# Kernel tuning notes

Measured on AMD Instinct MI355X. Metric: run time of the kernel, lower is better.

## Reference

```python
import jax, jax.numpy as jnp
import numpy as np


def setup_inputs() -> dict:
    key = jax.random.key(0)
    ks = jax.random.split(key, 7)
    bs, win_len, num_obj, d = 4, 64, 36, 2048
    s = 1.0 / np.sqrt(d)
    return {
        "region_feats": jax.random.normal(ks[0], (bs, win_len, num_obj, d), jnp.float32),
        "Wq": jax.random.normal(ks[1], (d, d), jnp.float32) * s,
        "bq": jax.random.normal(ks[2], (d,), jnp.float32) * 0.01,
        "Wk": jax.random.normal(ks[3], (d, d), jnp.float32) * s,
        "bk": jax.random.normal(ks[4], (d,), jnp.float32) * 0.01,
        "Wu": jax.random.normal(ks[5], (d, 1024), jnp.float32) * s,
        "bu": jax.random.normal(ks[6], (1024,), jnp.float32) * 0.01,
    }


def reference(region_feats, Wq, bq, Wk, bk, Wu, bu):
    bs, win_len, num_obj, d = region_feats.shape
    feats = region_feats.reshape(bs, win_len * num_obj, d)  # [b, n, d]
    q = feats @ Wq + bq                                     # [b, n, d]
    k = feats @ Wk + bk                                     # [b, n, d]
    adj = jnp.einsum('bnd,bmd->bnm', q, k)                  # unscaled QK^T, [b, n, n]
    adj_norm = jax.nn.softmax(adj, axis=-1)
    v = feats @ Wu + bu                                     # [b, n, 1024]
    out = jnp.einsum('bnm,bmv->bnv', adj_norm, v)
    return out.reshape(bs, win_len, num_obj, -1)
```

## Files before the change

kernel.cpp:

```cpp
#include <hip/hip_runtime.h>


typedef unsigned short u16;
typedef unsigned int   u32;
typedef signed char    i8;
typedef _Float16 f16;
typedef f16    f16x8 __attribute__((ext_vector_type(8)));
typedef float  f32x4 __attribute__((ext_vector_type(4)));
typedef int    i32x4 __attribute__((ext_vector_type(4)));
typedef u32    u32x4 __attribute__((ext_vector_type(4)));
typedef u16    u16x4 __attribute__((ext_vector_type(4)));

#define WAIT_VM0_LGKM0 0x0070

__device__ __forceinline__ void gload16(const void* g, void* l) {
    __builtin_amdgcn_global_load_lds(
        (const __attribute__((address_space(1))) unsigned int*)g,
        (__attribute__((address_space(3))) unsigned int*)l, 16, 0, 0);
}

__device__ __forceinline__ void tile_swizzle(int& tx, int& ty) {
    const int gx = gridDim.x, gy = gridDim.y;
    const int lin = blockIdx.y * gx + blockIdx.x;
    const int G = 4;
    const int gid = lin / (G * gx);
    const int g0 = gid * G;
    const int gh = min(G, gy - g0);
    const int rem = lin - gid * (G * gx);
    ty = g0 + rem % gh;
    tx = rem / gh;
}

__device__ __forceinline__ void digits256(float v, float s, i8& d1, i8& d0) {
    float f = fminf(fmaxf(v * s, -32600.0f), 32600.0f);
    int r = __float2int_rn(f);
    int a1 = (r + 128) >> 8;
    int a0 = r - (a1 << 8);
    d1 = (i8)a1;
    d0 = (i8)a0;
}

template <int EPI>
__device__ __forceinline__ void gemm_i8_body(
    i8* ldsb, int tx, int ty, int z,
    const i8* __restrict__ Ah, const i8* __restrict__ Al,
    const i8* __restrict__ Bh, const i8* __restrict__ Bl,
    i8* __restrict__ Qh, i8* __restrict__ Ql, float* __restrict__ Cf,
    float oscale, int N, int K, long strA, long strB, long strC) {
    const int tid  = threadIdx.x;
    const int lane = tid & 63;
    const int wv   = tid >> 6;
    const int wm   = wv >> 1, wn = wv & 1;
    const int l16  = lane & 15, kq = lane >> 4;
    const long rowBase = (long)ty * 128;
    const long colBase = (long)tx * 128;

    const i8* pAh = Ah + (long)z * strA;
    const i8* pAl = Al + (long)z * strA;
    const i8* pBh = Bh + (long)z * strB;
    const i8* pBl = Bl + (long)z * strB;

    const int l4r = lane >> 2, l4c = lane & 3;
    int rin[2];
    u32 voffA[2], voffB[2];
    int ldsoff[2];
    #pragma unroll
    for (int h = 0; h < 2; ++h) {
        rin[h] = h * 64 + wv * 16 + l4r;
        const int kw = (l4c - (rin[h] >> 1)) & 3;
        voffA[h] = (u32)((rowBase + rin[h]) * (long)K) + kw * 16;
        voffB[h] = (u32)((colBase + rin[h]) * (long)K) + kw * 16;
        ldsoff[h] = (h * 64 + wv * 16) * 64;
    }

    int aoff[4], boff[4];
    #pragma unroll
    for (int i = 0; i < 4; ++i) {
        const int rA = wm * 64 + i * 16 + l16;
        aoff[i] = rA * 64 + ((kq + (rA >> 1)) & 3) * 16;
        const int rB = wn * 64 + i * 16 + l16;
        boff[i] = rB * 64 + ((kq + (rB >> 1)) & 3) * 16;
    }

    const i32x4 izero = {0, 0, 0, 0};
    i32x4 ahh[4][4], acx[4][4], all_[4][4];
    #pragma unroll
    for (int i = 0; i < 4; ++i)
        #pragma unroll
        for (int j = 0; j < 4; ++j) { ahh[i][j] = izero; acx[i][j] = izero; all_[i][j] = izero; }

    const int nk = K >> 6;

    #pragma unroll
    for (int h = 0; h < 2; ++h) {
        gload16(pAh + voffA[h], ldsb         + ldsoff[h]);
        gload16(pAl + voffA[h], ldsb + 8192  + ldsoff[h]);
        gload16(pBh + voffB[h], ldsb + 16384 + ldsoff[h]);
        gload16(pBl + voffB[h], ldsb + 24576 + ldsoff[h]);
    }

    for (int kt = 0; kt < nk; ++kt) {
        const int cur = kt & 1;
        __builtin_amdgcn_s_waitcnt(WAIT_VM0_LGKM0);
        __builtin_amdgcn_s_barrier();

        if (kt + 1 < nk) {
            const long ko = (long)(kt + 1) * 64;
            i8* nb = ldsb + (1 - cur) * 32768;
            #pragma unroll
            for (int h = 0; h < 2; ++h) {
                gload16(pAh + voffA[h] + ko, nb         + ldsoff[h]);
                gload16(pAl + voffA[h] + ko, nb + 8192  + ldsoff[h]);
                gload16(pBh + voffB[h] + ko, nb + 16384 + ldsoff[h]);
                gload16(pBl + voffB[h] + ko, nb + 24576 + ldsoff[h]);
            }
        }

        __builtin_amdgcn_s_setprio(1);
        const i8* base = ldsb + cur * 32768;
        i32x4 fbh[4], fbl[4];
        #pragma unroll
        for (int j = 0; j < 4; ++j) {
            fbh[j] = *(const i32x4*)(base + 16384 + boff[j]);
            fbl[j] = *(const i32x4*)(base + 24576 + boff[j]);
        }
        #pragma unroll
        for (int i = 0; i < 4; ++i) {
            i32x4 fah = *(const i32x4*)(base + aoff[i]);
            i32x4 fal = *(const i32x4*)(base + 8192 + aoff[i]);
            #pragma unroll
            for (int j = 0; j < 4; ++j)
                ahh[i][j]  = __builtin_amdgcn_mfma_i32_16x16x64_i8(fah, fbh[j], ahh[i][j], 0, 0, 0);
            #pragma unroll
            for (int j = 0; j < 4; ++j)
                acx[i][j]  = __builtin_amdgcn_mfma_i32_16x16x64_i8(fah, fbl[j], acx[i][j], 0, 0, 0);
            #pragma unroll
            for (int j = 0; j < 4; ++j)
                all_[i][j] = __builtin_amdgcn_mfma_i32_16x16x64_i8(fal, fbl[j], all_[i][j], 0, 0, 0);
            #pragma unroll
            for (int j = 0; j < 4; ++j)
                acx[i][j]  = __builtin_amdgcn_mfma_i32_16x16x64_i8(fal, fbh[j], acx[i][j], 0, 0, 0);
        }
        __builtin_amdgcn_s_setprio(0);
    }

    #pragma unroll
    for (int i = 0; i < 4; ++i) {
        const long gr0 = rowBase + wm * 64 + i * 16 + kq * 4;
        #pragma unroll
        for (int j = 0; j < 4; ++j) {
            const long gc = colBase + wn * 64 + j * 16 + l16;
            #pragma unroll
            for (int r = 0; r < 4; ++r) {
                const float comb = 65536.0f * (float)ahh[i][j][r] +
                                     256.0f * (float)acx[i][j][r] +
                                             (float)all_[i][j][r];
                const long o = (gr0 + r) * (long)N + gc;
                if constexpr (EPI == 0) {
                    i8 d1, d0;
                    digits256(comb, oscale, d1, d0);
                    Qh[o] = d1;
                    Ql[o] = d0;
                } else {
                    Cf[(long)z * strC + o] = comb * oscale;
                }
            }
        }
    }
}

template <int EPI>
__device__ __forceinline__ void gemm_f16_body(
    i8* ldsb, int tx, int ty, int z,
    const u16* __restrict__ A, const u16* __restrict__ B,
    u16* __restrict__ Ch, float* __restrict__ Cf,
    const float* __restrict__ bias,
    int N, int K, long strA, long strB, long strC) {
    const int tid  = threadIdx.x;
    const int lane = tid & 63;
    const int wv   = tid >> 6;
    const int wm   = wv >> 1, wn = wv & 1;
    const int l16  = lane & 15, kq = lane >> 4;
    const long rowBase = (long)ty * 128;
    const long colBase = (long)tx * 128;

    const u16* pA = A + (long)z * strA;
    const u16* pB = B + (long)z * strB;

    const int l4r = lane >> 2, l4c = lane & 3;
    u32 voffA[2], voffB[2];
    int ldsoff[2];
    #pragma unroll
    for (int h = 0; h < 2; ++h) {
        const int rin = h * 64 + wv * 16 + l4r;
        const int kw = (l4c - (rin >> 1)) & 3;
        voffA[h] = (u32)((rowBase + rin) * (long)K) + kw * 8;
        voffB[h] = (u32)((colBase + rin) * (long)K) + kw * 8;
        ldsoff[h] = (h * 64 + wv * 16) * 64;
    }
    int aoff[4], boff[4];
    #pragma unroll
    for (int i = 0; i < 4; ++i) {
        const int rA = wm * 64 + i * 16 + l16;
        aoff[i] = rA * 64 + ((kq + (rA >> 1)) & 3) * 16;
        const int rB = wn * 64 + i * 16 + l16;
        boff[i] = rB * 64 + ((kq + (rB >> 1)) & 3) * 16;
    }

    const f32x4 vzero = {0.f, 0.f, 0.f, 0.f};
    f32x4 acc[4][4];
    #pragma unroll
    for (int i = 0; i < 4; ++i)
        #pragma unroll
        for (int j = 0; j < 4; ++j) acc[i][j] = vzero;

    const int nk = K >> 5;

    #pragma unroll
    for (int h = 0; h < 2; ++h) {
        gload16(pA + voffA[h], ldsb        + ldsoff[h]);
        gload16(pB + voffB[h], ldsb + 8192 + ldsoff[h]);
    }

    for (int kt = 0; kt < nk; ++kt) {
        const int cur = kt & 1;
        __builtin_amdgcn_s_waitcnt(WAIT_VM0_LGKM0);
        __builtin_amdgcn_s_barrier();

        if (kt + 1 < nk) {
            const long ko = (long)(kt + 1) * 32;
            i8* nb = ldsb + (1 - cur) * 16384;
            #pragma unroll
            for (int h = 0; h < 2; ++h) {
                gload16(pA + voffA[h] + ko, nb        + ldsoff[h]);
                gload16(pB + voffB[h] + ko, nb + 8192 + ldsoff[h]);
            }
        }

        __builtin_amdgcn_s_setprio(1);
        const i8* base = ldsb + cur * 16384;
        f16x8 fa[4];
        #pragma unroll
        for (int i = 0; i < 4; ++i)
            fa[i] = __builtin_bit_cast(f16x8, *(const u32x4*)(base + aoff[i]));
        #pragma unroll
        for (int j = 0; j < 4; ++j) {
            f16x8 fb = __builtin_bit_cast(f16x8, *(const u32x4*)(base + 8192 + boff[j]));
            #pragma unroll
            for (int i = 0; i < 4; ++i)
                acc[i][j] = __builtin_amdgcn_mfma_f32_16x16x32_f16(fa[i], fb, acc[i][j], 0, 0, 0);
        }
        __builtin_amdgcn_s_setprio(0);
    }

    #pragma unroll
    for (int i = 0; i < 4; ++i) {
        const long gr0 = rowBase + wm * 64 + i * 16 + kq * 4;
        #pragma unroll
        for (int j = 0; j < 4; ++j) {
            const long gc = colBase + wn * 64 + j * 16 + l16;
            f32x4 a = acc[i][j];
            if constexpr (EPI == 2) {
                const int b  = (int)(gr0 / 2304);
                const int n0 = (int)(gr0 - (long)b * 2304);
                u16x4 o4;
                #pragma unroll
                for (int r = 0; r < 4; ++r) o4[r] = __builtin_bit_cast(u16, (f16)a[r]);
                *(u16x4*)&Ch[(long)b * (1024L * 2304) + gc * 2304 + n0] = o4;
            } else {
                float* C = Cf + (long)z * strC;
                const float bv = bias[gc];
                #pragma unroll
                for (int r = 0; r < 4; ++r) C[(gr0 + r) * (long)N + gc] = a[r] + bv;
            }
        }
    }
}

__device__ __forceinline__ void quantFc_body(long row, float* red,
                                             const float* __restrict__ F,
                                             const float* __restrict__ u,
                                             u16* __restrict__ F16,
                                             i8* __restrict__ hi,
                                             i8* __restrict__ lo,
                                             float* __restrict__ c) {
    const int tid = threadIdx.x;
    const float* fr = F + row * 2048;
    float dot = 0.f;
    #pragma unroll
    for (int t = 0; t < 8; ++t) {
        const int i = t * 256 + tid;
        const float v = fr[i];
        F16[row * 2048 + i] = __builtin_bit_cast(u16, (f16)v);
        i8 d1, d0;
        digits256(v, 5440.0f, d1, d0);
        hi[row * 2048 + i] = d1;
        lo[row * 2048 + i] = d0;
        dot += v * u[i];
    }
    #pragma unroll
    for (int off = 32; off >= 1; off >>= 1) dot += __shfl_down(dot, off);
    if ((tid & 63) == 0) red[tid >> 6] = dot;
    __syncthreads();
    if (tid == 0) c[row] = red[0] + red[1] + red[2] + red[3];
}

__global__ __launch_bounds__(256) void prep_k(const float* __restrict__ Wk,
                                              const float* __restrict__ bq,
                                              float* __restrict__ u,
                                              const float* __restrict__ Wq,
                                              i8* __restrict__ Wqh, i8* __restrict__ Wql,
                                              i8* __restrict__ Wkh, i8* __restrict__ Wkl,
                                              const float* __restrict__ Wu,
                                              u16* __restrict__ WuT) {
    __shared__ __align__(16) float sm[32 * 33];
    const int tid = threadIdx.x;
    const int id = blockIdx.x;
    if (id < 2048) {
        const float* ar = Wk + (long)id * 2048;
        float s = 0.f;
        #pragma unroll
        for (int t = 0; t < 8; ++t) s += ar[t * 256 + tid] * bq[t * 256 + tid];
        #pragma unroll
        for (int off = 32; off >= 1; off >>= 1) s += __shfl_down(s, off);
        if ((tid & 63) == 0) sm[tid >> 6] = s;
        __syncthreads();
        if (tid == 0) u[id] = sm[0] + sm[1] + sm[2] + sm[3];
    } else if (id < 4096) {
        const int w  = id - 2048;
        const int bx = (w & 31) * 32;
        const int by = (w >> 5) * 32;
        const int lx = tid & 31, ly = tid >> 5;
        float (*t)[33] = (float (*)[33])sm;
        #pragma unroll
        for (int dy = 0; dy < 32; dy += 8)
            t[ly + dy][lx] = Wu[(long)(by + ly + dy) * 1024 + bx + lx];
        __syncthreads();
        #pragma unroll
        for (int dy = 0; dy < 32; dy += 8)
            WuT[(long)(bx + ly + dy) * 2048 + by + lx] =
                __builtin_bit_cast(u16, (f16)t[lx][ly + dy]);
    } else {
        long j = (long)id - 4096;
        const float* src;
        i8 *dh, *dl;
        if (j < 16384) { src = Wq; dh = Wqh; dl = Wql; }
        else           { j -= 16384; src = Wk; dh = Wkh; dl = Wkl; }
        const long i = j * 256 + tid;
        i8 d1, d0;
        digits256(src[i], 261120.0f, d1, d0);
        dh[i] = d1;
        dl[i] = d0;
    }
}

__global__ __launch_bounds__(256, 2) void fused_qfc_mt(
    const float* __restrict__ F, const float* __restrict__ u,
    u16* __restrict__ F16, i8* __restrict__ Fh, i8* __restrict__ Fl,
    float* __restrict__ c,
    const i8* __restrict__ Wqh, const i8* __restrict__ Wql,
    const i8* __restrict__ Wkh, const i8* __restrict__ Wkl,
    i8* __restrict__ Mth, i8* __restrict__ Mtl) {
    __shared__ __align__(16) i8 lds[2][32768];
    const int b = blockIdx.x;
    if (b < 256) {
        gemm_i8_body<0>(&lds[0][0], b & 15, b >> 4, 0,
                        Wkh, Wkl, Wqh, Wql, Mth, Mtl, nullptr,
                        3.8296569e-06f, 2048, 2048, 0L, 0L, 0L);
    } else {
        quantFc_body((long)b - 256, (float*)&lds[0][0], F, u, F16, Fh, Fl, c);
    }
}

__global__ __launch_bounds__(256, 2) void fused_sv(
    const i8* __restrict__ Fh, const i8* __restrict__ Fl,
    const i8* __restrict__ Mth, const i8* __restrict__ Mtl,
    i8* __restrict__ Sh, i8* __restrict__ Sl,
    const u16* __restrict__ F16, const u16* __restrict__ WuT,
    u16* __restrict__ vT) {
    __shared__ __align__(16) i8 lds[2][32768];
    const int bx = blockIdx.x, by = blockIdx.y;
    if (bx < 16) {
        gemm_i8_body<0>(&lds[0][0], bx, by, 0,
                        Fh, Fl, Mth, Mtl, Sh, Sl, nullptr,
                        3.8296569e-06f, 2048, 2048, 0L, 0L, 0L);
    } else {
        gemm_f16_body<2>(&lds[0][0], bx - 16, by, 0,
                         F16, WuT, vT, nullptr, nullptr,
                         1024, 2048, 0L, 0L, 0L);
    }
}

template <int EPI>
__global__ __launch_bounds__(256, 2) void gemm_i8_k(
    const i8* __restrict__ Ah, const i8* __restrict__ Al,
    const i8* __restrict__ Bh, const i8* __restrict__ Bl,
    i8* __restrict__ Qh, i8* __restrict__ Ql, float* __restrict__ Cf,
    float oscale, int N, int K, long strA, long strB, long strC) {
    __shared__ __align__(16) i8 lds[2][32768];
    int tx, ty;
    tile_swizzle(tx, ty);
    gemm_i8_body<EPI>(&lds[0][0], tx, ty, blockIdx.z,
                      Ah, Al, Bh, Bl, Qh, Ql, Cf, oscale, N, K, strA, strB, strC);
}

template <int EPI>
__global__ __launch_bounds__(256, 3) void gemm_f16_k(
    const u16* __restrict__ A, const u16* __restrict__ B,
    u16* __restrict__ Ch, float* __restrict__ Cf,
    const float* __restrict__ bias,
    int N, int K, long strA, long strB, long strC) {
    __shared__ __align__(16) i8 lds[2][16384];
    int tx, ty;
    tile_swizzle(tx, ty);
    gemm_f16_body<EPI>(&lds[0][0], tx, ty, blockIdx.z,
                       A, B, Ch, Cf, bias, N, K, strA, strB, strC);
}

__global__ __launch_bounds__(256) void softmax_k(const float* __restrict__ adj,
                                                 const float* __restrict__ c,
                                                 u16* __restrict__ P) {
    const int n = 2304;
    const int row = blockIdx.x, b = blockIdx.y;
    const int tid = threadIdx.x;
    const float* ar = adj + ((long)b * n + row) * (long)n;
    const float* cb = c + (long)b * n;
    u16* pr = P + ((long)b * n + row) * (long)n;

    float v[9];
    float mx = -3.0e38f;
    #pragma unroll
    for (int t = 0; t < 9; ++t) {
        const int i = t * 256 + tid;
        const float x = ar[i] + cb[i];
        v[t] = x;
        mx = fmaxf(mx, x);
    }
    #pragma unroll
    for (int off = 32; off >= 1; off >>= 1) mx = fmaxf(mx, __shfl_down(mx, off));
    __shared__ float red[4];
    if ((tid & 63) == 0) red[tid >> 6] = mx;
    __syncthreads();
    mx = fmaxf(fmaxf(red[0], red[1]), fmaxf(red[2], red[3]));

    float s = 0.f;
    #pragma unroll
    for (int t = 0; t < 9; ++t) {
        const float e = __expf(v[t] - mx);
        v[t] = e;
        s += e;
    }
    #pragma unroll
    for (int off = 32; off >= 1; off >>= 1) s += __shfl_down(s, off);
    __shared__ float red2[4];
    if ((tid & 63) == 0) red2[tid >> 6] = s;
    __syncthreads();
    s = red2[0] + red2[1] + red2[2] + red2[3];
    const float inv = 1.0f / s;
    #pragma unroll
    for (int t = 0; t < 9; ++t)
        pr[t * 256 + tid] = __builtin_bit_cast(u16, (f16)(v[t] * inv));
}

extern "C" void kernel_launch(void* const* d_in, const int* in_sizes, int n_in,
                              void* d_out, int out_size, void* d_ws, size_t ws_size,
                              hipStream_t stream) {
    (void)in_sizes; (void)n_in; (void)out_size; (void)ws_size;
    const float* F  = (const float*)d_in[0];
    const float* Wq = (const float*)d_in[1];
    const float* bq = (const float*)d_in[2];
    const float* Wk = (const float*)d_in[3];
    const float* Wu = (const float*)d_in[5];
    const float* bu = (const float*)d_in[6];
    float* out = (float*)d_out;

    char* ws = (char*)d_ws;
    const long o_F16  = 0L;
    const long o_Fh8  = 37748736L;
    const long o_Fl8  = 56623104L;
    const long o_Sh8  = 75497472L;
    const long o_Sl8  = 94371840L;
    const long o_adj  = 113246208L;
    const long o_P    = 198180864L;
    const long o_vT   = 240648192L;
    const long o_WuT  = 259522560L;
    const long o_Wqh  = 263716864L;
    const long o_Wql  = 267911168L;
    const long o_Wkh  = 272105472L;
    const long o_Wkl  = 276299776L;
    const long o_Mth  = 280494080L;
    const long o_Mtl  = 284688384L;
    const long o_u    = 288882688L;
    const long o_c    = 288890880L;

    u16* F16 = (u16*)(ws + o_F16);
    i8*  Fh8 = (i8*)(ws + o_Fh8);   i8* Fl8 = (i8*)(ws + o_Fl8);
    i8*  Sh8 = (i8*)(ws + o_Sh8);   i8* Sl8 = (i8*)(ws + o_Sl8);
    float* adj = (float*)(ws + o_adj);
    u16* P   = (u16*)(ws + o_P);
    u16* vT  = (u16*)(ws + o_vT);
    u16* WuT = (u16*)(ws + o_WuT);
    i8*  Wqh = (i8*)(ws + o_Wqh);   i8* Wql = (i8*)(ws + o_Wql);
    i8*  Wkh = (i8*)(ws + o_Wkh);   i8* Wkl = (i8*)(ws + o_Wkl);
    i8*  Mth = (i8*)(ws + o_Mth);   i8* Mtl = (i8*)(ws + o_Mtl);
    float* u = (float*)(ws + o_u);
    float* c = (float*)(ws + o_c);

    prep_k<<<36864, 256, 0, stream>>>(Wk, bq, u, Wq, Wqh, Wql, Wkh, Wkl, Wu, WuT);

    fused_qfc_mt<<<9472, 256, 0, stream>>>(F, u, F16, Fh8, Fl8, c,
                                           Wqh, Wql, Wkh, Wkl, Mth, Mtl);

    fused_sv<<<dim3(24, 72, 1), 256, 0, stream>>>(Fh8, Fl8, Mth, Mtl, Sh8, Sl8,
                                                  F16, WuT, vT);

    gemm_i8_k<1><<<dim3(18, 18, 4), 256, 0, stream>>>(
        Sh8, Sl8, Fh8, Fl8, nullptr, nullptr, adj,
        3.3791083e-08f, 2304, 2048,
        2304L * 2048, 2304L * 2048, 2304L * 2304);

    softmax_k<<<dim3(2304, 4, 1), 256, 0, stream>>>(adj, c, P);

    gemm_f16_k<3><<<dim3(8, 18, 4), 256, 0, stream>>>(
        P, vT, nullptr, out, bu, 1024, 2304,
        2304L * 2304, 1024L * 2304, 2304L * 1024);
}
```

Baseline: 624.0 us.

## Triple-buffer A tiles to prefetch two k-steps ahead in GEMM bodies

```diff
diff --git a/kernel.cpp b/kernel.cpp
--- a/kernel.cpp
+++ b/kernel.cpp
@@ -11,6 +11,8 @@
 typedef u32    u32x4 __attribute__((ext_vector_type(4)));
 typedef u16    u16x4 __attribute__((ext_vector_type(4)));
 
+#define WAIT_VM4_LGKM0 0x0074
+#define WAIT_VM2_LGKM0 0x0072
 #define WAIT_VM0_LGKM0 0x0070
 
 __device__ __forceinline__ void gload16(const void* g, void* l) {
@@ -91,43 +93,50 @@
 
     const int nk = K >> 6;
 
-    #pragma unroll
-    for (int h = 0; h < 2; ++h) {
-        gload16(pAh + voffA[h], ldsb         + ldsoff[h]);
-        gload16(pAl + voffA[h], ldsb + 8192  + ldsoff[h]);
-        gload16(pBh + voffB[h], ldsb + 16384 + ldsoff[h]);
-        gload16(pBl + voffB[h], ldsb + 24576 + ldsoff[h]);
-    }
+    auto issueA = [&](int j) {
+        i8* nb = ldsb + (j % 3) * 16384;
+        const long ko = (long)j * 64;
+        #pragma unroll
+        for (int h = 0; h < 2; ++h) {
+            gload16(pAh + voffA[h] + ko, nb        + ldsoff[h]);
+            gload16(pAl + voffA[h] + ko, nb + 8192 + ldsoff[h]);
+        }
+    };
+    auto issueB = [&](int j) {
+        i8* nb = ldsb + 49152 + (j & 1) * 16384;
+        const long ko = (long)j * 64;
+        #pragma unroll
+        for (int h = 0; h < 2; ++h) {
+            gload16(pBh + voffB[h] + ko, nb        + ldsoff[h]);
+            gload16(pBl + voffB[h] + ko, nb + 8192 + ldsoff[h]);
+        }
+    };
+
+    issueB(0);
+    issueA(0);
+    if (1 < nk) issueA(1);
 
     for (int kt = 0; kt < nk; ++kt) {
-        const int cur = kt & 1;
-        __builtin_amdgcn_s_waitcnt(WAIT_VM0_LGKM0);
+        if (kt == nk - 1) __builtin_amdgcn_s_waitcnt(WAIT_VM0_LGKM0);
+        else              __builtin_amdgcn_s_waitcnt(WAIT_VM4_LGKM0);
         __builtin_amdgcn_s_barrier();
 
-        if (kt + 1 < nk) {
-            const long ko = (long)(kt + 1) * 64;
-            i8* nb = ldsb + (1 - cur) * 32768;
-            #pragma unroll
-            for (int h = 0; h < 2; ++h) {
-                gload16(pAh + voffA[h] + ko, nb         + ldsoff[h]);
-                gload16(pAl + voffA[h] + ko, nb + 8192  + ldsoff[h]);
-                gload16(pBh + voffB[h] + ko, nb + 16384 + ldsoff[h]);
-                gload16(pBl + voffB[h] + ko, nb + 24576 + ldsoff[h]);
-            }
-        }
+        if (kt + 1 < nk) issueB(kt + 1);
+        if (kt + 2 < nk) issueA(kt + 2);
 
         __builtin_amdgcn_s_setprio(1);
-        const i8* base = ldsb + cur * 32768;
+        const i8* baseA = ldsb + (kt % 3) * 16384;
+        const i8* baseB = ldsb + 49152 + (kt & 1) * 16384;
         i32x4 fbh[4], fbl[4];
         #pragma unroll
         for (int j = 0; j < 4; ++j) {
-            fbh[j] = *(const i32x4*)(base + 16384 + boff[j]);
-            fbl[j] = *(const i32x4*)(base + 24576 + boff[j]);
+            fbh[j] = *(const i32x4*)(baseB + boff[j]);
+            fbl[j] = *(const i32x4*)(baseB + 8192 + boff[j]);
         }
         #pragma unroll
         for (int i = 0; i < 4; ++i) {
-            i32x4 fah = *(const i32x4*)(base + aoff[i]);
-            i32x4 fal = *(const i32x4*)(base + 8192 + aoff[i]);
+            i32x4 fah = *(const i32x4*)(baseA + aoff[i]);
+            i32x4 fal = *(const i32x4*)(baseA + 8192 + aoff[i]);
             #pragma unroll
             for (int j = 0; j < 4; ++j)
                 ahh[i][j]  = __builtin_amdgcn_mfma_i32_16x16x64_i8(fah, fbh[j], ahh[i][j], 0, 0, 0);
@@ -216,36 +225,43 @@
 
     const int nk = K >> 5;
 
-    #pragma unroll
-    for (int h = 0; h < 2; ++h) {
-        gload16(pA + voffA[h], ldsb        + ldsoff[h]);
-        gload16(pB + voffB[h], ldsb + 8192 + ldsoff[h]);
-    }
+    auto issueA = [&](int j) {
+        i8* nb = ldsb + (j % 3) * 8192;
+        const long ko = (long)j * 32;
+        #pragma unroll
+        for (int h = 0; h < 2; ++h)
+            gload16(pA + voffA[h] + ko, nb + ldsoff[h]);
+    };
+    auto issueB = [&](int j) {
+        i8* nb = ldsb + 24576 + (j & 1) * 8192;
+        const long ko = (long)j * 32;
+        #pragma unroll
+        for (int h = 0; h < 2; ++h)
+            gload16(pB + voffB[h] + ko, nb + ldsoff[h]);
+    };
+
+    issueB(0);
+    issueA(0);
+    if (1 < nk) issueA(1);
 
     for (int kt = 0; kt < nk; ++kt) {
-        const int cur = kt & 1;
-        __builtin_amdgcn_s_waitcnt(WAIT_VM0_LGKM0);
+        if (kt == nk - 1) __builtin_amdgcn_s_waitcnt(WAIT_VM0_LGKM0);
+        else              __builtin_amdgcn_s_waitcnt(WAIT_VM2_LGKM0);
         __builtin_amdgcn_s_barrier();
 
-        if (kt + 1 < nk) {
-            const long ko = (long)(kt + 1) * 32;
-            i8* nb = ldsb + (1 - cur) * 16384;
-            #pragma unroll
-            for (int h = 0; h < 2; ++h) {
-                gload16(pA + voffA[h] + ko, nb        + ldsoff[h]);
-                gload16(pB + voffB[h] + ko, nb + 8192 + ldsoff[h]);
-            }
-        }
+        if (kt + 1 < nk) issueB(kt + 1);
+        if (kt + 2 < nk) issueA(kt + 2);
 
         __builtin_amdgcn_s_setprio(1);
-        const i8* base = ldsb + cur * 16384;
+        const i8* baseA = ldsb + (kt % 3) * 8192;
+        const i8* baseB = ldsb + 24576 + (kt & 1) * 8192;
         f16x8 fa[4];
         #pragma unroll
         for (int i = 0; i < 4; ++i)
-            fa[i] = __builtin_bit_cast(f16x8, *(const u32x4*)(base + aoff[i]));
+            fa[i] = __builtin_bit_cast(f16x8, *(const u32x4*)(baseA + aoff[i]));
         #pragma unroll
         for (int j = 0; j < 4; ++j) {
-            f16x8 fb = __builtin_bit_cast(f16x8, *(const u32x4*)(base + 8192 + boff[j]));
+            f16x8 fb = __builtin_bit_cast(f16x8, *(const u32x4*)(baseB + boff[j]));
             #pragma unroll
             for (int i = 0; i < 4; ++i)
                 acc[i][j] = __builtin_amdgcn_mfma_f32_16x16x32_f16(fa[i], fb, acc[i][j], 0, 0, 0);
@@ -361,14 +377,14 @@
     const i8* __restrict__ Wqh, const i8* __restrict__ Wql,
     const i8* __restrict__ Wkh, const i8* __restrict__ Wkl,
     i8* __restrict__ Mth, i8* __restrict__ Mtl) {
-    __shared__ __align__(16) i8 lds[2][32768];
+    __shared__ __align__(16) i8 lds[81920];
     const int b = blockIdx.x;
     if (b < 256) {
-        gemm_i8_body<0>(&lds[0][0], b & 15, b >> 4, 0,
+        gemm_i8_body<0>(&lds[0], b & 15, b >> 4, 0,
                         Wkh, Wkl, Wqh, Wql, Mth, Mtl, nullptr,
                         3.8296569e-06f, 2048, 2048, 0L, 0L, 0L);
     } else {
-        quantFc_body((long)b - 256, (float*)&lds[0][0], F, u, F16, Fh, Fl, c);
+        quantFc_body((long)b - 256, (float*)&lds[0], F, u, F16, Fh, Fl, c);
     }
 }
 
@@ -378,14 +394,14 @@
     i8* __restrict__ Sh, i8* __restrict__ Sl,
     const u16* __restrict__ F16, const u16* __restrict__ WuT,
     u16* __restrict__ vT) {
-    __shared__ __align__(16) i8 lds[2][32768];
+    __shared__ __align__(16) i8 lds[81920];
     const int bx = blockIdx.x, by = blockIdx.y;
     if (bx < 16) {
-        gemm_i8_body<0>(&lds[0][0], bx, by, 0,
+        gemm_i8_body<0>(&lds[0], bx, by, 0,
                         Fh, Fl, Mth, Mtl, Sh, Sl, nullptr,
                         3.8296569e-06f, 2048, 2048, 0L, 0L, 0L);
     } else {
-        gemm_f16_body<2>(&lds[0][0], bx - 16, by, 0,
+        gemm_f16_body<2>(&lds[0], bx - 16, by, 0,
                          F16, WuT, vT, nullptr, nullptr,
                          1024, 2048, 0L, 0L, 0L);
     }
@@ -397,10 +413,10 @@
     const i8* __restrict__ Bh, const i8* __restrict__ Bl,
     i8* __restrict__ Qh, i8* __restrict__ Ql, float* __restrict__ Cf,
     float oscale, int N, int K, long strA, long strB, long strC) {
-    __shared__ __align__(16) i8 lds[2][32768];
+    __shared__ __align__(16) i8 lds[81920];
     int tx, ty;
     tile_swizzle(tx, ty);
-    gemm_i8_body<EPI>(&lds[0][0], tx, ty, blockIdx.z,
+    gemm_i8_body<EPI>(&lds[0], tx, ty, blockIdx.z,
                       Ah, Al, Bh, Bl, Qh, Ql, Cf, oscale, N, K, strA, strB, strC);
 }
 
@@ -410,10 +426,10 @@
     u16* __restrict__ Ch, float* __restrict__ Cf,
     const float* __restrict__ bias,
     int N, int K, long strA, long strB, long strC) {
-    __shared__ __align__(16) i8 lds[2][16384];
+    __shared__ __align__(16) i8 lds[40960];
     int tx, ty;
     tile_swizzle(tx, ty);
-    gemm_f16_body<EPI>(&lds[0][0], tx, ty, blockIdx.z,
+    gemm_f16_body<EPI>(&lds[0], tx, ty, blockIdx.z,
                        A, B, Ch, Cf, bias, N, K, strA, strB, strC);
 }
 
```

Measured after the change: 636.8 us. 2.1% more time.
